# Kernel tuning notes

Hardware: AMD Instinct MI355X
Metric: run time of the kernel (lower is better)

## Reference

```python
import jax, jax.numpy as jnp
import numpy as np

N_NODES = 100000
N_EDGES = 1600000
NUM_GRAPHS = 4096
HID = 128
F_IN = 11
F_OUT = 19


def setup_inputs() -> dict:
    key = jax.random.key(0)
    ks = jax.random.split(key, 8)
    x = jax.random.normal(ks[0], (N_NODES, F_IN), dtype=jnp.float32)
    edge_src = jax.random.randint(ks[1], (N_EDGES,), 0, N_NODES)
    edge_dst = jax.random.randint(ks[2], (N_EDGES,), 0, N_NODES)
    batch = jnp.sort(jax.random.randint(ks[3], (N_NODES,), 0, NUM_GRAPHS))
    W1 = jax.random.normal(ks[4], (F_IN, HID), dtype=jnp.float32) / np.sqrt(F_IN)
    b1 = jnp.zeros((HID,), dtype=jnp.float32)
    W2 = jax.random.normal(ks[5], (HID, HID), dtype=jnp.float32) / np.sqrt(HID)
    b2 = jnp.zeros((HID,), dtype=jnp.float32)
    Wlin = jax.random.normal(ks[6], (HID, F_OUT), dtype=jnp.float32) / np.sqrt(HID)
    blin = jnp.zeros((F_OUT,), dtype=jnp.float32)
    return {"x": x, "edge_src": edge_src, "edge_dst": edge_dst, "batch": batch,
            "W1": W1, "b1": b1, "W2": W2, "b2": b2, "Wlin": Wlin, "blin": blin}


def _gcn_conv(x, W, b, src, dst, norm, n_nodes):
    # x: [N, Fin] -> h: [N, Fout]; gather-normalize-scatter over edges (self-loops included in src/dst/norm)
    h = x @ W
    msgs = h[src] * norm[:, None]              # [E+N, Fout]
    out = jax.ops.segment_sum(msgs, dst, num_segments=n_nodes)
    return out + b


def reference(x, edge_src, edge_dst, batch, W1, b1, W2, b2, Wlin, blin):
    n = x.shape[0]
    # add self-loops (GCNConv default)
    loops = jnp.arange(n)
    src = jnp.concatenate([edge_src, loops])
    dst = jnp.concatenate([edge_dst, loops])
    # symmetric normalization deg^-1/2[src] * deg^-1/2[dst], deg computed on dst with self-loops
    deg = jax.ops.segment_sum(jnp.ones_like(dst, dtype=x.dtype), dst, num_segments=n)
    dinv = jnp.where(deg > 0, jax.lax.rsqrt(deg), 0.0)
    norm = dinv[src] * dinv[dst]
    h = _gcn_conv(x, W1, b1, src, dst, norm, n)
    h = jax.nn.relu(h)
    h = _gcn_conv(h, W2, b2, src, dst, norm, n)
    # global mean pool over batch assignment
    sums = jax.ops.segment_sum(h, batch, num_segments=NUM_GRAPHS)
    cnts = jax.ops.segment_sum(jnp.ones((n,), dtype=h.dtype), batch, num_segments=NUM_GRAPHS)
    pooled = sums / jnp.maximum(cnts, 1.0)[:, None]   # [NUM_GRAPHS, HID]
    return pooled @ Wlin + blin                       # [NUM_GRAPHS, F_OUT]
```

## Files before the change

### kernel.cpp

```cpp
#include <hip/hip_runtime.h>
#include <hip/hip_fp16.h>

#define N_NODES 100000
#define N_EDGES 1600000
#define NUM_G   4096
#define HID     128
#define F_IN    11
#define F_PAD   16
#define F_OUT   19

#define NB      256
#define KPB     391
#define BCAP    8192
#define GCAP    1024
#define P01_EPB 2048
#define NREG    8
#define REGW    12500
#define GPB     4
#define NAGG    782
#define CH_G    8

__device__ inline void acc_row_f16(float* acc, uint4 u, float w) {
    const __half2* hp = (const __half2*)&u;
#pragma unroll
    for (int i = 0; i < 4; ++i) {
        acc[2 * i]     += __half2float(__low2half(hp[i]))  * w;
        acc[2 * i + 1] += __half2float(__high2half(hp[i])) * w;
    }
}
__device__ inline void add_row_f16(float* acc, uint4 u) {
    const __half2* hp = (const __half2*)&u;
#pragma unroll
    for (int i = 0; i < 4; ++i) {
        acc[2 * i]     += __half2float(__low2half(hp[i]));
        acc[2 * i + 1] += __half2float(__high2half(hp[i]));
    }
}

__global__ void p1_place(const int* __restrict__ src, const int* __restrict__ dst,
                         int* __restrict__ bcur, unsigned int* __restrict__ ebuf) {
    __shared__ int h[NB];
    __shared__ int lbase[NB];
    __shared__ int gbase[NB];
    __shared__ int wsum4[4];
    __shared__ int total_s;
    __shared__ unsigned int stage[P01_EPB];
    __shared__ unsigned char sbuck[P01_EPB];
    int tid = threadIdx.x;
    h[tid] = 0;
    __syncthreads();
    unsigned int pk[8]; int bn[8];
    int b0 = blockIdx.x * P01_EPB;
    int e8 = b0 + tid * 8;
    if (e8 + 8 <= N_EDGES) {
        int4 s0 = *(const int4*)(src + e8);
        int4 s1 = *(const int4*)(src + e8 + 4);
        int4 d0 = *(const int4*)(dst + e8);
        int4 d1 = *(const int4*)(dst + e8 + 4);
        int ss[8] = { s0.x, s0.y, s0.z, s0.w, s1.x, s1.y, s1.z, s1.w };
        int dd[8] = { d0.x, d0.y, d0.z, d0.w, d1.x, d1.y, d1.z, d1.w };
#pragma unroll
        for (int k = 0; k < 8; ++k) {
            bn[k] = dd[k] / KPB;
            pk[k] = ((unsigned)ss[k] << 9) | (unsigned)(dd[k] - bn[k] * KPB);
        }
    } else {
#pragma unroll
        for (int k = 0; k < 8; ++k) {
            int e = e8 + k;
            if (e < N_EDGES) {
                int d = dst[e];
                bn[k] = d / KPB;
                pk[k] = ((unsigned)src[e] << 9) | (unsigned)(d - bn[k] * KPB);
            } else bn[k] = -1;
        }
    }
#pragma unroll
    for (int k = 0; k < 8; ++k)
        if (bn[k] >= 0) atomicAdd(&h[bn[k]], 1);
    __syncthreads();
    int c = h[tid];
    gbase[tid] = c ? atomicAdd(&bcur[tid], c) : 0;
    int lane = tid & 63, wv = tid >> 6;
    int sv = c;
#pragma unroll
    for (int off = 1; off < 64; off <<= 1) {
        int n = __shfl_up(sv, off, 64);
        if (lane >= off) sv += n;
    }
    if (lane == 63) wsum4[wv] = sv;
    __syncthreads();
    int woff = 0;
    for (int w = 0; w < wv; ++w) woff += wsum4[w];
    int excl = sv - c + woff;
    lbase[tid] = excl;
    if (tid == NB - 1) total_s = excl + c;
    __syncthreads();
    h[tid] = 0;
    __syncthreads();
#pragma unroll
    for (int k = 0; k < 8; ++k) {
        if (bn[k] >= 0) {
            int r = atomicAdd(&h[bn[k]], 1);
            int p_ = lbase[bn[k]] + r;
            stage[p_] = pk[k];
            sbuck[p_] = (unsigned char)bn[k];
        }
    }
    __syncthreads();
    int total = total_s;
    for (int i = tid; i < total; i += NB) {
        int b = sbuck[i];
        ebuf[(size_t)b * BCAP + gbase[b] + (i - lbase[b])] = stage[i];
    }
}

__global__ void p2_build(const unsigned int* __restrict__ ebuf, const int* __restrict__ bcur,
                         const float* __restrict__ x,
                         int* __restrict__ row_ptr, int* __restrict__ deg,
                         int* __restrict__ col, float* __restrict__ wd,
                         float* __restrict__ dinv, __half* __restrict__ xp) {
    __shared__ int hist[512];
    __shared__ float ldinv[512];
    __shared__ int wsum[8];
    __shared__ int woff[8];
    int b  = blockIdx.x;
    int t  = threadIdx.x;
    int dbase = b * KPB;
    int nd = N_NODES - dbase; if (nd > KPB) nd = KPB;
    if (t < 512) hist[t] = 0;
    __syncthreads();
    int e0 = b * BCAP;
    int e1 = e0 + bcur[b];
    for (int e = e0 + t; e < e1; e += 1024)
        atomicAdd(&hist[ebuf[e] & 511u], 1);
    __syncthreads();
    int v = 0, sv = 0;
    int lane = t & 63, wv = t >> 6;
    if (t < 512) {
        v = hist[t];
        sv = v;
#pragma unroll
        for (int off = 1; off < 64; off <<= 1) {
            int n = __shfl_up(sv, off, 64);
            if (lane >= off) sv += n;
        }
        if (lane == 63) wsum[wv] = sv;
    }
    __syncthreads();
    if (t == 0) {
        int run = 0;
#pragma unroll
        for (int w = 0; w < 8; ++w) { woff[w] = run; run += wsum[w]; }
    }
    __syncthreads();
    int excl = 0;
    if (t < 512) {
        excl = sv - v + woff[wv];
        float di = rsqrtf(1.0f + (float)v);
        ldinv[t] = di;
        if (t < nd) {
            row_ptr[dbase + t] = e0 + excl;
            deg[dbase + t]     = v;
            dinv[dbase + t]    = di;
        }
    }
    __syncthreads();
    if (t < 512) hist[t] = e0 + excl;
    __syncthreads();
    for (int e = e0 + t; e < e1; e += 1024) {
        unsigned int w = ebuf[e];
        int dl = (int)(w & 511u);
        int pos = atomicAdd(&hist[dl], 1);
        col[pos] = (int)(w >> 9);
        wd[pos]  = ldinv[dl];
    }
    for (int idx = t; idx < nd * F_PAD; idx += 1024) {
        int vl = idx >> 4, f = idx & 15;
        int gv = dbase + vl;
        xp[(size_t)gv * F_PAD + f] =
            __float2half_rn((f < F_IN) ? ldinv[vl] * x[(size_t)gv * F_IN + f] : 0.f);
    }
}

__global__ void agg_es8(const __half* __restrict__ xp, const int* __restrict__ row_ptr,
                        const int* __restrict__ deg, const int* __restrict__ col,
                        const float* __restrict__ dinv,
                        const float* __restrict__ W1, const float* __restrict__ b1,
                        __half* __restrict__ Bh,
                        const int* __restrict__ batch, const float* __restrict__ wd,
                        uint2* __restrict__ ewp, int* __restrict__ gro,
                        int* __restrict__ gb) {
    __shared__ float xs[128][F_PAD];
    __shared__ float W1s[F_IN * HID];
    __shared__ float b1s[HID];
    __shared__ float ds[128];
    __shared__ int cnt[NREG];
    __shared__ int cur[NREG];
    __shared__ int range[2];
    int tid = threadIdx.x;

    if (blockIdx.x < NAGG) {
        for (int i = tid; i < F_IN * HID; i += 256) W1s[i] = W1[i];
        if (tid < HID) b1s[tid] = b1[tid];
        const uint4* xp4 = (const uint4*)xp;
        int v0   = blockIdx.x * 128;
        int v    = v0 + (tid >> 1);
        int lane = tid & 1;
        if (v < N_NODES) {
            if (lane == 0) ds[tid >> 1] = dinv[v];
            float a[8];
#pragma unroll
            for (int k = 0; k < 8; ++k) a[k] = 0.f;
            add_row_f16(a, xp4[(size_t)v * 2 + lane]);
            int j = row_ptr[v], end = j + deg[v];
            for (; j + 3 < end; j += 4) {
                int s0 = col[j], s1 = col[j + 1], s2 = col[j + 2], s3 = col[j + 3];
                uint4 u0 = xp4[(size_t)s0 * 2 + lane];
                uint4 u1 = xp4[(size_t)s1 * 2 + lane];
                uint4 u2 = xp4[(size_t)s2 * 2 + lane];
                uint4 u3 = xp4[(size_t)s3 * 2 + lane];
                add_row_f16(a, u0); add_row_f16(a, u1);
                add_row_f16(a, u2); add_row_f16(a, u3);
            }
            for (; j < end; ++j)
                add_row_f16(a, xp4[(size_t)col[j] * 2 + lane]);
#pragma unroll
            for (int k = 0; k < 8; ++k) xs[tid >> 1][lane * 8 + k] = a[k];
        }
        __syncthreads();
        int jf   = tid & 127;
        int half = tid >> 7;
        int nmax = N_NODES - v0; if (nmax > 128) nmax = 128;
        for (int n = half; n < nmax; n += 2) {
            float a = 0.f;
#pragma unroll
            for (int k = 0; k < F_IN; ++k) a += xs[n][k] * W1s[k * HID + jf];
            float dv = ds[n];
            float h = fmaxf(dv * a + b1s[jf], 0.f);
            Bh[(size_t)(v0 + n) * HID + jf] = __float2half_rn(dv * h);
        }
    } else {
        int g = blockIdx.x - NAGG;
        if (tid < NREG) cnt[tid] = 0;
        if (tid < 2) {
            int tgt = g + tid;
            int lo = 0, hi = N_NODES;
            while (lo < hi) { int m = (lo + hi) >> 1; if (batch[m] < tgt) lo = m + 1; else hi = m; }
            range[tid] = lo;
        }
        __syncthreads();
        int r0 = range[0], r1 = range[1];
        if (tid == 0) {
            gb[g] = r0;
            if (g == NUM_G - 1) gb[NUM_G] = N_NODES;
        }
        int bb0 = 0, bb1 = -1;
        if (r1 > r0) { bb0 = r0 / KPB; bb1 = (r1 - 1) / KPB; }
        for (int bb = bb0; bb <= bb1; ++bb) {
            int vlo = r0 > bb * KPB ? r0 : bb * KPB;
            int vhi = r1 < bb * KPB + KPB ? r1 : bb * KPB + KPB;
            int ee0 = row_ptr[vlo];
            int ee1 = row_ptr[vhi - 1] + deg[vhi - 1];
            for (int e = ee0 + tid; e < ee1; e += 256)
                atomicAdd(&cnt[(unsigned)col[e] / REGW], 1);
        }
        for (int v = r0 + tid; v < r1; v += 256)
            atomicAdd(&cnt[(unsigned)v / REGW], 1);
        __syncthreads();
        if (tid == 0) {
            int run = g * GCAP;
#pragma unroll
            for (int p = 0; p < NREG; ++p) {
                gro[g * 9 + p] = run;
                cur[p] = run;
                run += cnt[p];
            }
            gro[g * 9 + 8] = run;
        }
        __syncthreads();
        for (int bb = bb0; bb <= bb1; ++bb) {
            int vlo = r0 > bb * KPB ? r0 : bb * KPB;
            int vhi = r1 < bb * KPB + KPB ? r1 : bb * KPB + KPB;
            int ee0 = row_ptr[vlo];
            int ee1 = row_ptr[vhi - 1] + deg[vhi - 1];
            for (int e = ee0 + tid; e < ee1; e += 256) {
                int s = col[e];
                int pos = atomicAdd(&cur[(unsigned)s / REGW], 1);
                ewp[pos] = make_uint2((unsigned)s, __float_as_uint(wd[e]));
            }
        }
        for (int v = r0 + tid; v < r1; v += 256) {
            int pos = atomicAdd(&cur[(unsigned)v / REGW], 1);
            ewp[pos] = make_uint2((unsigned)v, __float_as_uint(dinv[v]));
        }
    }
}

__global__ void pool_gather(const __half* __restrict__ Bh,
                            const int* __restrict__ gro,
                            const uint2* __restrict__ ewp,
                            float* __restrict__ part) {
    __shared__ float red[32][HID + 4];
    int b    = blockIdx.x;
    int gset = b >> 3;
    int p    = b & 7;
    int tid  = threadIdx.x;
    int grp  = tid >> 3;
    int lane = tid & 7;
    int g    = gset * GPB + (grp >> 3);
    int q    = grp & 7;
    const uint4* B4 = (const uint4*)Bh;
    float acc[16];
#pragma unroll
    for (int k = 0; k < 16; ++k) acc[k] = 0.f;

    int e0 = gro[g * 9 + p], e1 = gro[g * 9 + p + 1];
    int e = e0 + q;
    for (; e + 24 < e1; e += 32) {
        uint2 q0 = ewp[e], q1 = ewp[e + 8], q2 = ewp[e + 16], q3 = ewp[e + 24];
        uint4 u00 = B4[(size_t)q0.x * 16 + lane];
        uint4 u01 = B4[(size_t)q0.x * 16 + 8 + lane];
        uint4 u10 = B4[(size_t)q1.x * 16 + lane];
        uint4 u11 = B4[(size_t)q1.x * 16 + 8 + lane];
        uint4 u20 = B4[(size_t)q2.x * 16 + lane];
        uint4 u21 = B4[(size_t)q2.x * 16 + 8 + lane];
        uint4 u30 = B4[(size_t)q3.x * 16 + lane];
        uint4 u31 = B4[(size_t)q3.x * 16 + 8 + lane];
        float w0 = __uint_as_float(q0.y), w1 = __uint_as_float(q1.y);
        float w2 = __uint_as_float(q2.y), w3 = __uint_as_float(q3.y);
        acc_row_f16(acc,     u00, w0);
        acc_row_f16(acc + 8, u01, w0);
        acc_row_f16(acc,     u10, w1);
        acc_row_f16(acc + 8, u11, w1);
        acc_row_f16(acc,     u20, w2);
        acc_row_f16(acc + 8, u21, w2);
        acc_row_f16(acc,     u30, w3);
        acc_row_f16(acc + 8, u31, w3);
    }
    for (; e < e1; e += 8) {
        uint2 q0 = ewp[e];
        uint4 u00 = B4[(size_t)q0.x * 16 + lane];
        uint4 u01 = B4[(size_t)q0.x * 16 + 8 + lane];
        float w0 = __uint_as_float(q0.y);
        acc_row_f16(acc,     u00, w0);
        acc_row_f16(acc + 8, u01, w0);
    }
#pragma unroll
    for (int k = 0; k < 8; ++k) red[grp][lane * 8 + k]      = acc[k];
#pragma unroll
    for (int k = 0; k < 8; ++k) red[grp][64 + lane * 8 + k] = acc[8 + k];
    __syncthreads();
    for (int i = tid; i < GPB * HID; i += 256) {
        int gg = i >> 7, f = i & 127;
        int rb = gg * 8;
        float s = 0.f;
#pragma unroll
        for (int r = 0; r < 8; ++r) s += red[rb + r][f];
        part[(size_t)((gset * GPB + gg) * NREG + p) * HID + f] = s;
    }
}

__global__ void combine_head(const float* __restrict__ part, const int* __restrict__ gb,
                             const float* __restrict__ W2, const float* __restrict__ b2,
                             const float* __restrict__ Wlin, const float* __restrict__ blin,
                             float* __restrict__ out) {
    __shared__ float r[CH_G][HID];
    __shared__ float tt[CH_G][HID + 4];
    __shared__ float bsc[CH_G];
    int g0  = blockIdx.x * CH_G;
    int tid = threadIdx.x;
    int f   = tid & 127;
    int gh  = tid >> 7;
    int q0  = gh * 4;
#pragma unroll
    for (int c = 0; c < 4; ++c) {
        int gg = q0 + c;
        int g  = g0 + gg;
        float s = 0.f;
#pragma unroll
        for (int p = 0; p < NREG; ++p) s += part[(size_t)(g * NREG + p) * HID + f];
        int cnt = gb[g + 1] - gb[g];
        float inv = (cnt > 0) ? 1.0f / (float)cnt : 0.f;
        r[gg][f] = s * inv;
        if (f == 0) bsc[gg] = (cnt > 0) ? 1.0f : 0.f;
    }
    __syncthreads();
    float bf = b2[f];
    float t0 = bf * bsc[q0];
    float t1 = bf * bsc[q0 + 1];
    float t2 = bf * bsc[q0 + 2];
    float t3 = bf * bsc[q0 + 3];
#pragma unroll 4
    for (int k = 0; k < HID; ++k) {
        float w = W2[k * HID + f];
        t0 += r[q0][k] * w;
        t1 += r[q0 + 1][k] * w;
        t2 += r[q0 + 2][k] * w;
        t3 += r[q0 + 3][k] * w;
    }
    tt[q0][f]     = t0;
    tt[q0 + 1][f] = t1;
    tt[q0 + 2][f] = t2;
    tt[q0 + 3][f] = t3;
    __syncthreads();
    if (tid < CH_G * F_OUT) {
        int gg = tid / F_OUT;
        int fo = tid - gg * F_OUT;
        float o = blin[fo];
#pragma unroll 8
        for (int k = 0; k < HID; ++k) o += tt[gg][k] * Wlin[k * F_OUT + fo];
        out[(size_t)(g0 + gg) * F_OUT + fo] = o;
    }
}

extern "C" void kernel_launch(void* const* d_in, const int* in_sizes, int n_in,
                              void* d_out, int out_size, void* d_ws, size_t ws_size,
                              hipStream_t stream) {
    const float* x    = (const float*)d_in[0];
    const int*   esrc = (const int*)  d_in[1];
    const int*   edst = (const int*)  d_in[2];
    const int*   batch= (const int*)  d_in[3];
    const float* W1   = (const float*)d_in[4];
    const float* b1   = (const float*)d_in[5];
    const float* W2   = (const float*)d_in[6];
    const float* b2   = (const float*)d_in[7];
    const float* Wlin = (const float*)d_in[8];
    const float* blin = (const float*)d_in[9];
    float* out = (float*)d_out;

    char* p = (char*)d_ws;
    float*        dinv    = (float*)p;        p += sizeof(float) * N_NODES;
    __half*       xp      = (__half*)p;       p += sizeof(__half) * (size_t)N_NODES * F_PAD;
    __half*       Bh      = (__half*)p;       p += sizeof(__half) * (size_t)N_NODES * HID;
    unsigned int* ebuf    = (unsigned int*)p; p += sizeof(unsigned int) * (size_t)NB * BCAP;
    int*          col     = (int*)p;          p += sizeof(int) * (size_t)NB * BCAP;
    float*        wd      = (float*)p;        p += sizeof(float) * (size_t)NB * BCAP;
    int*          deg     = (int*)p;          p += sizeof(int) * N_NODES;
    uint2*        ewp     = (uint2*)p;        p += sizeof(uint2) * (size_t)NUM_G * GCAP;
    float*        part    = (float*)p;        p += sizeof(float) * (size_t)NUM_G * NREG * HID;
    int*          row_ptr = (int*)p;          p += sizeof(int) * (N_NODES + 4);
    int*          gb      = (int*)p;          p += sizeof(int) * (NUM_G + 4);
    int*          gro     = (int*)p;          p += sizeof(int) * (NUM_G * 9 + 4);
    int*          bcur    = (int*)p;          p += sizeof(int) * NB;

    const int nblk_e = (N_EDGES + P01_EPB - 1) / P01_EPB;

    hipMemsetAsync(bcur, 0, sizeof(int) * NB, stream);
    p1_place<<<nblk_e, 256, 0, stream>>>(esrc, edst, bcur, ebuf);
    p2_build<<<NB, 1024, 0, stream>>>(ebuf, bcur, x, row_ptr, deg, col, wd, dinv, xp);

    agg_es8<<<NAGG + NUM_G, 256, 0, stream>>>(xp, row_ptr, deg, col, dinv, W1, b1, Bh,
                                              batch, wd, ewp, gro, gb);

    pool_gather<<<(NUM_G / GPB) * NREG, 256, 0, stream>>>(Bh, gro, ewp, part);

    combine_head<<<NUM_G / CH_G, 256, 0, stream>>>(part, gb, W2, b2, Wlin, blin, out);
}
```

Baseline: 230.0 us.

## Interleave col/weight into uint2 CSR, hoist graph-boundary search, shrink pool unroll

```diff
diff --git a/kernel.cpp b/kernel.cpp
--- a/kernel.cpp
+++ b/kernel.cpp
@@ -14,6 +14,8 @@
 #define BCAP    8192
 #define GCAP    1024
 #define P01_EPB 2048
+#define NBLK_E  782
+#define NGBB    16
 #define NREG    8
 #define REGW    12500
 #define GPB     4
@@ -38,7 +40,19 @@
 }
 
 __global__ void p1_place(const int* __restrict__ src, const int* __restrict__ dst,
-                         int* __restrict__ bcur, unsigned int* __restrict__ ebuf) {
+                         const int* __restrict__ batch,
+                         int* __restrict__ bcur, unsigned int* __restrict__ ebuf,
+                         int* __restrict__ gb) {
+    if (blockIdx.x >= NBLK_E) {
+        int g = (blockIdx.x - NBLK_E) * 256 + threadIdx.x;
+        if (g < NUM_G) {
+            int lo = 0, hi = N_NODES;
+            while (lo < hi) { int m = (lo + hi) >> 1; if (batch[m] < g) lo = m + 1; else hi = m; }
+            gb[g] = lo;
+            if (g == NUM_G - 1) gb[NUM_G] = N_NODES;
+        }
+        return;
+    }
     __shared__ int h[NB];
     __shared__ int lbase[NB];
     __shared__ int gbase[NB];
@@ -118,7 +132,7 @@
 __global__ void p2_build(const unsigned int* __restrict__ ebuf, const int* __restrict__ bcur,
                          const float* __restrict__ x,
                          int* __restrict__ row_ptr, int* __restrict__ deg,
-                         int* __restrict__ col, float* __restrict__ wd,
+                         uint2* __restrict__ cw,
                          float* __restrict__ dinv, __half* __restrict__ xp) {
     __shared__ int hist[512];
     __shared__ float ldinv[512];
@@ -172,8 +186,7 @@
         unsigned int w = ebuf[e];
         int dl = (int)(w & 511u);
         int pos = atomicAdd(&hist[dl], 1);
-        col[pos] = (int)(w >> 9);
-        wd[pos]  = ldinv[dl];
+        cw[pos] = make_uint2(w >> 9, __float_as_uint(ldinv[dl]));
     }
     for (int idx = t; idx < nd * F_PAD; idx += 1024) {
         int vl = idx >> 4, f = idx & 15;
@@ -184,20 +197,18 @@
 }
 
 __global__ void agg_es8(const __half* __restrict__ xp, const int* __restrict__ row_ptr,
-                        const int* __restrict__ deg, const int* __restrict__ col,
+                        const int* __restrict__ deg, const uint2* __restrict__ cw,
                         const float* __restrict__ dinv,
                         const float* __restrict__ W1, const float* __restrict__ b1,
                         __half* __restrict__ Bh,
-                        const int* __restrict__ batch, const float* __restrict__ wd,
-                        uint2* __restrict__ ewp, int* __restrict__ gro,
-                        int* __restrict__ gb) {
+                        const int* __restrict__ gb,
+                        uint2* __restrict__ ewp, int* __restrict__ gro) {
     __shared__ float xs[128][F_PAD];
     __shared__ float W1s[F_IN * HID];
     __shared__ float b1s[HID];
     __shared__ float ds[128];
     __shared__ int cnt[NREG];
     __shared__ int cur[NREG];
-    __shared__ int range[2];
     int tid = threadIdx.x;
 
     if (blockIdx.x < NAGG) {
@@ -215,7 +226,7 @@
             add_row_f16(a, xp4[(size_t)v * 2 + lane]);
             int j = row_ptr[v], end = j + deg[v];
             for (; j + 3 < end; j += 4) {
-                int s0 = col[j], s1 = col[j + 1], s2 = col[j + 2], s3 = col[j + 3];
+                int s0 = cw[j].x, s1 = cw[j + 1].x, s2 = cw[j + 2].x, s3 = cw[j + 3].x;
                 uint4 u0 = xp4[(size_t)s0 * 2 + lane];
                 uint4 u1 = xp4[(size_t)s1 * 2 + lane];
                 uint4 u2 = xp4[(size_t)s2 * 2 + lane];
@@ -224,7 +235,7 @@
                 add_row_f16(a, u2); add_row_f16(a, u3);
             }
             for (; j < end; ++j)
-                add_row_f16(a, xp4[(size_t)col[j] * 2 + lane]);
+                add_row_f16(a, xp4[(size_t)cw[j].x * 2 + lane]);
 #pragma unroll
             for (int k = 0; k < 8; ++k) xs[tid >> 1][lane * 8 + k] = a[k];
         }
@@ -243,18 +254,8 @@
     } else {
         int g = blockIdx.x - NAGG;
         if (tid < NREG) cnt[tid] = 0;
-        if (tid < 2) {
-            int tgt = g + tid;
-            int lo = 0, hi = N_NODES;
-            while (lo < hi) { int m = (lo + hi) >> 1; if (batch[m] < tgt) lo = m + 1; else hi = m; }
-            range[tid] = lo;
-        }
         __syncthreads();
-        int r0 = range[0], r1 = range[1];
-        if (tid == 0) {
-            gb[g] = r0;
-            if (g == NUM_G - 1) gb[NUM_G] = N_NODES;
-        }
+        int r0 = gb[g], r1 = gb[g + 1];
         int bb0 = 0, bb1 = -1;
         if (r1 > r0) { bb0 = r0 / KPB; bb1 = (r1 - 1) / KPB; }
         for (int bb = bb0; bb <= bb1; ++bb) {
@@ -263,7 +264,7 @@
             int ee0 = row_ptr[vlo];
             int ee1 = row_ptr[vhi - 1] + deg[vhi - 1];
             for (int e = ee0 + tid; e < ee1; e += 256)
-                atomicAdd(&cnt[(unsigned)col[e] / REGW], 1);
+                atomicAdd(&cnt[cw[e].x / REGW], 1);
         }
         for (int v = r0 + tid; v < r1; v += 256)
             atomicAdd(&cnt[(unsigned)v / REGW], 1);
@@ -285,9 +286,9 @@
             int ee0 = row_ptr[vlo];
             int ee1 = row_ptr[vhi - 1] + deg[vhi - 1];
             for (int e = ee0 + tid; e < ee1; e += 256) {
-                int s = col[e];
-                int pos = atomicAdd(&cur[(unsigned)s / REGW], 1);
-                ewp[pos] = make_uint2((unsigned)s, __float_as_uint(wd[e]));
+                uint2 q = cw[e];
+                int pos = atomicAdd(&cur[q.x / REGW], 1);
+                ewp[pos] = q;
             }
         }
         for (int v = r0 + tid; v < r1; v += 256) {
@@ -317,26 +318,17 @@
 
     int e0 = gro[g * 9 + p], e1 = gro[g * 9 + p + 1];
     int e = e0 + q;
-    for (; e + 24 < e1; e += 32) {
-        uint2 q0 = ewp[e], q1 = ewp[e + 8], q2 = ewp[e + 16], q3 = ewp[e + 24];
+    for (; e + 8 < e1; e += 16) {
+        uint2 q0 = ewp[e], q1 = ewp[e + 8];
         uint4 u00 = B4[(size_t)q0.x * 16 + lane];
         uint4 u01 = B4[(size_t)q0.x * 16 + 8 + lane];
         uint4 u10 = B4[(size_t)q1.x * 16 + lane];
         uint4 u11 = B4[(size_t)q1.x * 16 + 8 + lane];
-        uint4 u20 = B4[(size_t)q2.x * 16 + lane];
-        uint4 u21 = B4[(size_t)q2.x * 16 + 8 + lane];
-        uint4 u30 = B4[(size_t)q3.x * 16 + lane];
-        uint4 u31 = B4[(size_t)q3.x * 16 + 8 + lane];
         float w0 = __uint_as_float(q0.y), w1 = __uint_as_float(q1.y);
-        float w2 = __uint_as_float(q2.y), w3 = __uint_as_float(q3.y);
         acc_row_f16(acc,     u00, w0);
         acc_row_f16(acc + 8, u01, w0);
         acc_row_f16(acc,     u10, w1);
         acc_row_f16(acc + 8, u11, w1);
-        acc_row_f16(acc,     u20, w2);
-        acc_row_f16(acc + 8, u21, w2);
-        acc_row_f16(acc,     u30, w3);
-        acc_row_f16(acc + 8, u31, w3);
     }
     for (; e < e1; e += 8) {
         uint2 q0 = ewp[e];
@@ -434,8 +426,7 @@
     __half*       xp      = (__half*)p;       p += sizeof(__half) * (size_t)N_NODES * F_PAD;
     __half*       Bh      = (__half*)p;       p += sizeof(__half) * (size_t)N_NODES * HID;
     unsigned int* ebuf    = (unsigned int*)p; p += sizeof(unsigned int) * (size_t)NB * BCAP;
-    int*          col     = (int*)p;          p += sizeof(int) * (size_t)NB * BCAP;
-    float*        wd      = (float*)p;        p += sizeof(float) * (size_t)NB * BCAP;
+    uint2*        cw      = (uint2*)p;        p += sizeof(uint2) * (size_t)NB * BCAP;
     int*          deg     = (int*)p;          p += sizeof(int) * N_NODES;
     uint2*        ewp     = (uint2*)p;        p += sizeof(uint2) * (size_t)NUM_G * GCAP;
     float*        part    = (float*)p;        p += sizeof(float) * (size_t)NUM_G * NREG * HID;
@@ -444,14 +435,12 @@
     int*          gro     = (int*)p;          p += sizeof(int) * (NUM_G * 9 + 4);
     int*          bcur    = (int*)p;          p += sizeof(int) * NB;
 
-    const int nblk_e = (N_EDGES + P01_EPB - 1) / P01_EPB;
-
     hipMemsetAsync(bcur, 0, sizeof(int) * NB, stream);
-    p1_place<<<nblk_e, 256, 0, stream>>>(esrc, edst, bcur, ebuf);
-    p2_build<<<NB, 1024, 0, stream>>>(ebuf, bcur, x, row_ptr, deg, col, wd, dinv, xp);
-
-    agg_es8<<<NAGG + NUM_G, 256, 0, stream>>>(xp, row_ptr, deg, col, dinv, W1, b1, Bh,
-                                              batch, wd, ewp, gro, gb);
+    p1_place<<<NBLK_E + NGBB, 256, 0, stream>>>(esrc, edst, batch, bcur, ebuf, gb);
+    p2_build<<<NB, 1024, 0, stream>>>(ebuf, bcur, x, row_ptr, deg, cw, dinv, xp);
+
+    agg_es8<<<NAGG + NUM_G, 256, 0, stream>>>(xp, row_ptr, deg, cw, dinv, W1, b1, Bh,
+                                              gb, ewp, gro);
 
     pool_gather<<<(NUM_G / GPB) * NREG, 256, 0, stream>>>(Bh, gro, ewp, part);
 
```

Result: faster. 207.4 us (-9.8%).
